# Kernel optimization log

Measured on AMD Instinct MI355X. Metric: run time of the kernel, lower is better.

The kernel has to match this reference:

```python
import jax, jax.numpy as jnp
import numpy as np

S, B, D, H = 512, 32, 1024, 16
HD = D // H
EPS = 1e-5


def layer_norm(x, w, b):
    xf = x.astype(jnp.float32)
    mu = jnp.mean(xf, axis=-1, keepdims=True)
    var = jnp.mean(jnp.square(xf - mu), axis=-1, keepdims=True)
    return ((xf - mu) * jax.lax.rsqrt(var + EPS) * w + b).astype(x.dtype)


def quick_gelu(x):
    return x * jax.nn.sigmoid(1.702 * x)


def setup_inputs() -> dict:
    key = jax.random.key(0)
    ks = jax.random.split(key, 6)
    sc = 0.02
    return {
        "x": jax.random.normal(ks[0], (S, B, D), dtype=jnp.float32),
        "ln1_w": jnp.ones((D,), jnp.float32),
        "ln1_b": jnp.zeros((D,), jnp.float32),
        "in_proj_w": jax.random.normal(ks[1], (3 * D, D), jnp.float32) * sc,
        "in_proj_b": jnp.zeros((3 * D,), jnp.float32),
        "out_w": jax.random.normal(ks[2], (D, D), jnp.float32) * sc,
        "out_b": jnp.zeros((D,), jnp.float32),
        "ln2_w": jnp.ones((D,), jnp.float32),
        "ln2_b": jnp.zeros((D,), jnp.float32),
        "fc_w": jax.random.normal(ks[3], (4 * D, D), jnp.float32) * sc,
        "fc_b": jnp.zeros((4 * D,), jnp.float32),
        "proj_w": jax.random.normal(ks[4], (D, 4 * D), jnp.float32) * sc,
        "proj_b": jnp.zeros((D,), jnp.float32),
    }


def reference(x, ln1_w, ln1_b, in_proj_w, in_proj_b, out_w, out_b,
              ln2_w, ln2_b, fc_w, fc_b, proj_w, proj_b):
    # ---- MHA on ln_1(x) (torch eager path, need_weights=True) ----
    h = layer_norm(x, ln1_w, ln1_b)                      # (S,B,D)
    qkv = h @ in_proj_w.T + in_proj_b                    # (S,B,3D)
    q, k, v = jnp.split(qkv, 3, axis=-1)
    # (S,B,D) -> (B,H,S,hd)
    def to_bhsd(t):
        return t.reshape(S, B, H, HD).transpose(1, 2, 0, 3)
    q, k, v = to_bhsd(q), to_bhsd(k), to_bhsd(v)
    scores = jnp.einsum('bhqd,bhkd->bhqk', q, k) / jnp.sqrt(jnp.float32(HD))
    attn = jax.nn.softmax(scores, axis=-1)               # (B,H,S,S)
    attn_weights = jnp.mean(attn, axis=1)                # avg over heads: (B,S,S)
    ctx = jnp.einsum('bhqk,bhkd->bhqd', attn, v)         # (B,H,S,hd)
    ctx = ctx.transpose(2, 0, 1, 3).reshape(S, B, D)     # (S,B,D)
    attn_out = ctx @ out_w.T + out_b
    x = x + attn_out
    # ---- MLP on ln_2(x) ----
    m = layer_norm(x, ln2_w, ln2_b)
    m = quick_gelu(m @ fc_w.T + fc_b)
    x = x + (m @ proj_w.T + proj_b)
    return x, attn_weights
```

## Files before the change

### kernel.cpp

```cpp
#include <hip/hip_runtime.h>
#include <hip/hip_bf16.h>

typedef __bf16 bf16x8 __attribute__((ext_vector_type(8)));
typedef __bf16 bf16x4 __attribute__((ext_vector_type(4)));
typedef float f32x4 __attribute__((ext_vector_type(4)));

#define SEQ 512
#define BATCH 32
#define DIM 1024
#define NHEAD 16
#define MROWS (SEQ * BATCH)

__device__ __forceinline__ void gload16(const void* g, void* s) {
    __builtin_amdgcn_global_load_lds((const __attribute__((address_space(1))) void*)g,
                                     (__attribute__((address_space(3))) void*)s, 16, 0, 0);
}

__device__ __forceinline__ f32x4 mfma16(bf16x8 a, bf16x8 b, f32x4 c) {
    return __builtin_amdgcn_mfma_f32_16x16x32_bf16(a, b, c, 0, 0, 0);
}

__global__ __launch_bounds__(256) void cvt_kernel(const float* __restrict__ src,
                                                  __bf16* __restrict__ dst, int n) {
    int i = (blockIdx.x * 256 + threadIdx.x) * 4;
    if (i < n) {
        float4 v = *(const float4*)(src + i);
        bf16x4 o;
        o[0] = (__bf16)v.x; o[1] = (__bf16)v.y; o[2] = (__bf16)v.z; o[3] = (__bf16)v.w;
        *(bf16x4*)&dst[i] = o;
    }
}

__global__ __launch_bounds__(256) void ln_kernel(const float* __restrict__ x,
                                                 const float* __restrict__ w,
                                                 const float* __restrict__ b,
                                                 __bf16* __restrict__ out) {
    int row = blockIdx.x, t = threadIdx.x;
    const float4* xr = (const float4*)(x + (size_t)row * DIM);
    float4 v = xr[t];
    float s  = v.x + v.y + v.z + v.w;
    float ss = v.x * v.x + v.y * v.y + v.z * v.z + v.w * v.w;
#pragma unroll
    for (int o = 1; o < 64; o <<= 1) { s += __shfl_xor(s, o); ss += __shfl_xor(ss, o); }
    __shared__ float red[8];
    if ((t & 63) == 0) { red[t >> 6] = s; red[4 + (t >> 6)] = ss; }
    __syncthreads();
    s  = red[0] + red[1] + red[2] + red[3];
    ss = red[4] + red[5] + red[6] + red[7];
    float mu = s * (1.f / DIM);
    float rs = rsqrtf(ss * (1.f / DIM) - mu * mu + 1e-5f);
    int c = t * 4;
    bf16x4 o4;
    o4[0] = (__bf16)((v.x - mu) * rs * w[c + 0] + b[c + 0]);
    o4[1] = (__bf16)((v.y - mu) * rs * w[c + 1] + b[c + 1]);
    o4[2] = (__bf16)((v.z - mu) * rs * w[c + 2] + b[c + 2]);
    o4[3] = (__bf16)((v.w - mu) * rs * w[c + 3] + b[c + 3]);
    *(bf16x4*)&out[(size_t)row * DIM + c] = o4;
}

template <int MODE>
__global__ __launch_bounds__(256) void gemm_kernel(const __bf16* __restrict__ A,
                                                   const __bf16* __restrict__ W,
                                                   const float* __restrict__ bias,
                                                   const float* res, void* out,
                                                   int M, int N, int K) {
    __shared__ __bf16 As[128 * 64];
    __shared__ __bf16 Bs[128 * 64];
    char* Ab_s = (char*)As;
    char* Bb_s = (char*)Bs;
    int t = threadIdx.x, l = t & 63, wv = t >> 6;
    int m0 = blockIdx.y * 128, n0 = blockIdx.x * 128;
    int wm = (wv >> 1) * 64, wn = (wv & 1) * 64;
    int lr = l & 15, lqb = (l >> 4) * 16;
    f32x4 acc[4][4];
#pragma unroll
    for (int i = 0; i < 4; i++)
#pragma unroll
        for (int j = 0; j < 4; j++) acc[i][j] = (f32x4){0.f, 0.f, 0.f, 0.f};

    const __bf16* Ag = A + (size_t)m0 * K;
    const __bf16* Wg = W + (size_t)n0 * K;
    int srow = t >> 3, sslot = t & 7;

    for (int k0 = 0; k0 < K; k0 += 64) {
#pragma unroll
        for (int it = 0; it < 4; ++it) {
            int row = it * 32 + srow;
            int col = (sslot ^ (row & 7)) * 8;
            int L = it * 4096 + t * 16;
            gload16(Ag + (size_t)row * K + k0 + col, Ab_s + L);
            gload16(Wg + (size_t)row * K + k0 + col, Bb_s + L);
        }
        __syncthreads();
#pragma unroll
        for (int f2 = 0; f2 < 2; ++f2) {
            bf16x8 af[4], bfr[4];
#pragma unroll
            for (int i = 0; i < 4; i++) {
                int row = wm + i * 16 + lr;
                af[i] = *(const bf16x8*)(Ab_s + row * 128 + ((f2 * 64 + lqb) ^ ((row & 7) << 4)));
            }
#pragma unroll
            for (int j = 0; j < 4; j++) {
                int row = wn + j * 16 + lr;
                bfr[j] = *(const bf16x8*)(Bb_s + row * 128 + ((f2 * 64 + lqb) ^ ((row & 7) << 4)));
            }
#pragma unroll
            for (int i = 0; i < 4; i++)
#pragma unroll
                for (int j = 0; j < 4; j++)
                    acc[i][j] = mfma16(af[i], bfr[j], acc[i][j]);
        }
        __syncthreads();
    }

#pragma unroll
    for (int j = 0; j < 4; j++) {
        int col = n0 + wn + j * 16 + lr;
        float bv = bias[col];
#pragma unroll
        for (int i = 0; i < 4; i++) {
#pragma unroll
            for (int r = 0; r < 4; r++) {
                int row = m0 + wm + i * 16 + (l >> 4) * 4 + r;
                float v = acc[i][j][r] + bv;
                if (MODE == 1) v = v / (1.f + __expf(-1.702f * v));
                size_t idx = (size_t)row * N + col;
                if (MODE == 2) ((float*)out)[idx] = v + res[idx];
                else           ((__bf16*)out)[idx] = (__bf16)v;
            }
        }
    }
}

__global__ __launch_bounds__(256) void vtr_kernel(const __bf16* __restrict__ qkv,
                                                  __bf16* __restrict__ Vt) {
    __shared__ __bf16 tl[64 * 72];
    char* tb = (char*)tl;
    int t = threadIdx.x;
    int bh = blockIdx.x >> 3, st = blockIdx.x & 7;
    int bb = bh >> 4, h = bh & 15;
#pragma unroll
    for (int it = 0; it < 2; ++it) {
        int s = it * 32 + (t >> 3), d0 = (t & 7) * 8;
        bf16x8 v = *(const bf16x8*)&qkv[((size_t)((st * 64 + s) * BATCH + bb)) * 3072 + 2048 + h * 64 + d0];
        *(bf16x8*)(tb + s * 144 + ((d0 * 2) ^ (((s + (s >> 3)) & 7) << 4))) = v;
    }
    __syncthreads();
#pragma unroll
    for (int it = 0; it < 2; ++it) {
        int d = it * 32 + (t >> 3), s0 = (t & 7) * 8;
        bf16x8 o;
#pragma unroll
        for (int e = 0; e < 8; ++e) {
            int s = s0 + e;
            o[e] = *(const __bf16*)(tb + s * 144 + ((d * 2) ^ (((s + (s >> 3)) & 7) << 4)));
        }
        *(bf16x8*)&Vt[((size_t)(bb * NHEAD + h) * 64 + d) * 512 + st * 64 + s0] = o;
    }
}

__global__ __launch_bounds__(512, 4) void attn_kernel(const __bf16* __restrict__ qkv,
                                                      const __bf16* __restrict__ Vt,
                                                      __bf16* __restrict__ ctx,
                                                      float* __restrict__ attnw) {
    __shared__ __bf16 kvbuf[16384];
    __shared__ __bf16 p16s[16384];
    __shared__ __bf16 qts[2048];
    __shared__ float redm[32][4];
    __shared__ float reds[32][4];
    char* kvb = (char*)kvbuf;
    char* pps = (char*)p16s;
    char* qtb = (char*)qts;

    const int t = threadIdx.x;
    const int l = t & 63, w = t >> 6;
    const int wq = w >> 2, wc = w & 3;
    const int lq = l >> 4, lr = l & 15;
    const int bb = blockIdx.x & 31;
    const int qt0 = blockIdx.x >> 5;

    const int ksl = t >> 3, kslot = t & 7;
    const int vdl = t >> 5, vslot = t & 31;

    float aw[8][4];
#pragma unroll
    for (int i = 0; i < 8; i++)
#pragma unroll
        for (int r = 0; r < 4; r++) aw[i][r] = 0.f;

    const int prow = wq * 16 + lr;
    const int vd = wc * 16 + lr;

    for (int h = 0; h < NHEAD; ++h) {
        if (t < 256) {
            int qr = t >> 3, slot = t & 7;
            int d0 = (slot ^ (qr & 7)) * 8;
            gload16(qkv + ((size_t)((qt0 * 32 + qr) * BATCH + bb)) * 3072 + h * 64 + d0,
                    qtb + t * 16);
        }
#pragma unroll
        for (int it = 0; it < 4; ++it) {
            int s = it * 64 + ksl;
            int d0 = (kslot ^ (s & 7)) * 8;
            gload16(qkv + ((size_t)(s * BATCH + bb)) * 3072 + 1024 + h * 64 + d0,
                    kvb + it * 8192 + t * 16);
        }
        __syncthreads();

        bf16x8 af0 = *(const bf16x8*)(qtb + prow * 128 + ((lq * 16) ^ ((prow & 7) << 4)));
        bf16x8 af1 = *(const bf16x8*)(qtb + prow * 128 + ((64 + lq * 16) ^ ((prow & 7) << 4)));

        f32x4 acc[8];
#pragma unroll
        for (int i = 0; i < 8; i++) acc[i] = (f32x4){0.f, 0.f, 0.f, 0.f};

#pragma unroll
        for (int ntl = 0; ntl < 4; ++ntl) {
            int r = wc * 64 + ntl * 16 + lr;
            bf16x8 b0 = *(const bf16x8*)(kvb + r * 128 + ((lq * 16) ^ ((r & 7) << 4)));
            bf16x8 b1 = *(const bf16x8*)(kvb + r * 128 + ((64 + lq * 16) ^ ((r & 7) << 4)));
            acc[ntl] = mfma16(af0, b0, acc[ntl]);
            acc[ntl] = mfma16(af1, b1, acc[ntl]);
        }
        __syncthreads();
#pragma unroll
        for (int it = 0; it < 4; ++it) {
            int s = it * 64 + ksl;
            int d0 = (kslot ^ (s & 7)) * 8;
            gload16(qkv + ((size_t)((256 + s) * BATCH + bb)) * 3072 + 1024 + h * 64 + d0,
                    kvb + it * 8192 + t * 16);
        }
        __syncthreads();
#pragma unroll
        for (int ntl = 0; ntl < 4; ++ntl) {
            int r = wc * 64 + ntl * 16 + lr;
            bf16x8 b0 = *(const bf16x8*)(kvb + r * 128 + ((lq * 16) ^ ((r & 7) << 4)));
            bf16x8 b1 = *(const bf16x8*)(kvb + r * 128 + ((64 + lq * 16) ^ ((r & 7) << 4)));
            acc[4 + ntl] = mfma16(af0, b0, acc[4 + ntl]);
            acc[4 + ntl] = mfma16(af1, b1, acc[4 + ntl]);
        }
        __syncthreads();
#pragma unroll
        for (int it = 0; it < 4; ++it) {
            int d = it * 16 + vdl;
            int s0 = (vslot ^ (d & 7)) * 8;
            gload16(Vt + ((size_t)(bb * NHEAD + h) * 64 + d) * 512 + s0,
                    kvb + it * 8192 + t * 16);
        }
#pragma unroll
        for (int i = 0; i < 8; i++) acc[i] *= 0.125f;
        float mx[4];
#pragma unroll
        for (int r = 0; r < 4; ++r) {
            float m = acc[0][r];
#pragma unroll
            for (int i = 1; i < 8; ++i) m = fmaxf(m, acc[i][r]);
#pragma unroll
            for (int o = 1; o < 16; o <<= 1) m = fmaxf(m, __shfl_xor(m, o));
            mx[r] = m;
        }
        if (lr == 0) {
            redm[wq * 16 + lq * 4 + 0][wc] = mx[0];
            redm[wq * 16 + lq * 4 + 1][wc] = mx[1];
            redm[wq * 16 + lq * 4 + 2][wc] = mx[2];
            redm[wq * 16 + lq * 4 + 3][wc] = mx[3];
        }
        __syncthreads();
        float g[4], sm[4];
#pragma unroll
        for (int r = 0; r < 4; ++r) {
            int row = wq * 16 + lq * 4 + r;
            g[r] = fmaxf(fmaxf(redm[row][0], redm[row][1]),
                         fmaxf(redm[row][2], redm[row][3]));
            sm[r] = 0.f;
        }
#pragma unroll
        for (int i = 0; i < 8; ++i)
#pragma unroll
            for (int r = 0; r < 4; ++r) {
                float p = __expf(acc[i][r] - g[r]);
                acc[i][r] = p;
                sm[r] += p;
            }
#pragma unroll
        for (int r = 0; r < 4; ++r)
#pragma unroll
            for (int o = 1; o < 16; o <<= 1) sm[r] += __shfl_xor(sm[r], o);
        if (lr == 0) {
            reds[wq * 16 + lq * 4 + 0][wc] = sm[0];
            reds[wq * 16 + lq * 4 + 1][wc] = sm[1];
            reds[wq * 16 + lq * 4 + 2][wc] = sm[2];
            reds[wq * 16 + lq * 4 + 3][wc] = sm[3];
        }
        __syncthreads();
        float inv[4];
#pragma unroll
        for (int r = 0; r < 4; ++r) {
            int row = wq * 16 + lq * 4 + r;
            inv[r] = 1.f / (reds[row][0] + reds[row][1] + reds[row][2] + reds[row][3]);
        }
#pragma unroll
        for (int i = 0; i < 8; ++i) {
#pragma unroll
            for (int r = 0; r < 4; ++r) {
                float pn = acc[i][r] * inv[r];
                aw[i][r] += pn;
                int row = wq * 16 + lq * 4 + r;
                int cbyte = (i >> 2) * 512 + wc * 128 + (i & 3) * 32 + lr * 2;
                *(__bf16*)(pps + row * 1024 + (cbyte ^ ((row & 7) << 4))) = (__bf16)pn;
            }
        }
        __syncthreads();
        f32x4 cacc = (f32x4){0.f, 0.f, 0.f, 0.f};
#pragma unroll
        for (int ks = 0; ks < 8; ++ks) {
            bf16x8 ap = *(const bf16x8*)(pps + prow * 1024 + ((ks * 64 + lq * 16) ^ ((prow & 7) << 4)));
            bf16x8 bv = *(const bf16x8*)(kvb + vd * 512 + ((ks * 64 + lq * 16) ^ ((vd & 7) << 4)));
            cacc = mfma16(ap, bv, cacc);
        }
        __syncthreads();
#pragma unroll
        for (int it = 0; it < 4; ++it) {
            int d = it * 16 + vdl;
            int s0 = (vslot ^ (d & 7)) * 8;
            gload16(Vt + ((size_t)(bb * NHEAD + h) * 64 + d) * 512 + 256 + s0,
                    kvb + it * 8192 + t * 16);
        }
        __syncthreads();
#pragma unroll
        for (int ks = 0; ks < 8; ++ks) {
            bf16x8 ap = *(const bf16x8*)(pps + prow * 1024 + ((512 + ks * 64 + lq * 16) ^ ((prow & 7) << 4)));
            bf16x8 bv = *(const bf16x8*)(kvb + vd * 512 + ((ks * 64 + lq * 16) ^ ((vd & 7) << 4)));
            cacc = mfma16(ap, bv, cacc);
        }
#pragma unroll
        for (int r = 0; r < 4; ++r) {
            int q = qt0 * 32 + wq * 16 + lq * 4 + r;
            ctx[((size_t)(q * BATCH + bb)) * DIM + h * 64 + wc * 16 + lr] = (__bf16)cacc[r];
        }
        __syncthreads();
    }
#pragma unroll
    for (int i = 0; i < 8; ++i)
#pragma unroll
        for (int r = 0; r < 4; ++r) {
            int q = qt0 * 32 + wq * 16 + lq * 4 + r;
            int col = (i >> 2) * 256 + wc * 64 + (i & 3) * 16 + lr;
            attnw[(size_t)bb * (SEQ * SEQ) + (size_t)q * SEQ + col] = aw[i][r] * (1.f / NHEAD);
        }
}

extern "C" void kernel_launch(void* const* d_in, const int* in_sizes, int n_in,
                              void* d_out, int out_size, void* d_ws, size_t ws_size,
                              hipStream_t stream) {
    const float* x    = (const float*)d_in[0];
    const float* ln1w = (const float*)d_in[1];
    const float* ln1b = (const float*)d_in[2];
    const float* ipw  = (const float*)d_in[3];
    const float* ipb  = (const float*)d_in[4];
    const float* outw = (const float*)d_in[5];
    const float* outb = (const float*)d_in[6];
    const float* ln2w = (const float*)d_in[7];
    const float* ln2b = (const float*)d_in[8];
    const float* fcw  = (const float*)d_in[9];
    const float* fcb  = (const float*)d_in[10];
    const float* pjw  = (const float*)d_in[11];
    const float* pjb  = (const float*)d_in[12];

    float* xout  = (float*)d_out;
    float* awout = xout + (size_t)MROWS * DIM;

    __bf16* wip   = (__bf16*)d_ws;
    __bf16* wout_ = wip + 3145728;
    __bf16* wfc   = wout_ + 1048576;
    __bf16* wpj   = wfc + 4194304;
    __bf16* hbuf  = wpj + 4194304;
    __bf16* big   = hbuf + (size_t)MROWS * DIM;
    __bf16* qkv   = big;
    __bf16* ctxb  = big + (size_t)MROWS * 3072;
    __bf16* mg    = big;
    __bf16* Vt    = hbuf;

    cvt_kernel<<<3072, 256, 0, stream>>>(ipw,  wip,   3145728);
    cvt_kernel<<<1024, 256, 0, stream>>>(outw, wout_, 1048576);
    cvt_kernel<<<4096, 256, 0, stream>>>(fcw,  wfc,   4194304);
    cvt_kernel<<<4096, 256, 0, stream>>>(pjw,  wpj,   4194304);

    ln_kernel<<<MROWS, 256, 0, stream>>>(x, ln1w, ln1b, hbuf);

    gemm_kernel<0><<<dim3(24, 128), 256, 0, stream>>>(hbuf, wip, ipb, nullptr, qkv,
                                                      MROWS, 3072, 1024);

    vtr_kernel<<<32 * 16 * 8, 256, 0, stream>>>(qkv, Vt);

    attn_kernel<<<512, 512, 0, stream>>>(qkv, Vt, ctxb, awout);

    gemm_kernel<2><<<dim3(8, 128), 256, 0, stream>>>(ctxb, wout_, outb, x, xout,
                                                     MROWS, 1024, 1024);

    ln_kernel<<<MROWS, 256, 0, stream>>>(xout, ln2w, ln2b, hbuf);

    gemm_kernel<1><<<dim3(32, 128), 256, 0, stream>>>(hbuf, wfc, fcb, nullptr, mg,
                                                      MROWS, 4096, 1024);

    gemm_kernel<2><<<dim3(8, 128), 256, 0, stream>>>(mg, wpj, pjb, xout, xout,
                                                     MROWS, 1024, 4096);
}
```

Before: 1.211 ms.

## Replace GEMM with 256x256 double-buffered 8-wave pipelined kernel

Replaces the 128x128 single-buffered GEMM with a 256x256-tile, 512-thread kernel. It double-buffers LDS (128 KB) and interleaves async global-to-LDS loads with MFMA phases, using explicit waitcnt, barriers and setprio. Block indices are swizzled across XCD groups to improve L2 locality. This is meant to hide memory latency and raise MFMA utilisation in all four linear layers. In exchange it needs more registers, leaves fewer blocks per CU, and relies on hand-tuned synchronisation that could be fragile.

```diff
diff --git a/kernel.cpp b/kernel.cpp
--- a/kernel.cpp
+++ b/kernel.cpp
@@ -58,72 +58,210 @@
     *(bf16x4*)&out[(size_t)row * DIM + c] = o4;
 }
 
+#define BA0 0
+#define BB0 32768
+#define BA1 65536
+#define BB1 98304
+
+#define PH_MID \
+    __builtin_amdgcn_s_barrier(); \
+    asm volatile("s_waitcnt lgkmcnt(0)" ::: "memory"); \
+    __builtin_amdgcn_sched_barrier(0); \
+    __builtin_amdgcn_s_setprio(1);
+#define PH_END \
+    __builtin_amdgcn_s_setprio(0); \
+    __builtin_amdgcn_sched_barrier(0); \
+    __builtin_amdgcn_s_barrier();
+#define PH_END_VM4 \
+    __builtin_amdgcn_s_setprio(0); \
+    __builtin_amdgcn_sched_barrier(0); \
+    asm volatile("s_waitcnt vmcnt(4)" ::: "memory"); \
+    __builtin_amdgcn_s_barrier();
+#define PH_END_VM0 \
+    __builtin_amdgcn_s_setprio(0); \
+    __builtin_amdgcn_sched_barrier(0); \
+    asm volatile("s_waitcnt vmcnt(0)" ::: "memory"); \
+    __builtin_amdgcn_s_barrier();
+
 template <int MODE>
-__global__ __launch_bounds__(256) void gemm_kernel(const __bf16* __restrict__ A,
-                                                   const __bf16* __restrict__ W,
-                                                   const float* __restrict__ bias,
-                                                   const float* res, void* out,
-                                                   int M, int N, int K) {
-    __shared__ __bf16 As[128 * 64];
-    __shared__ __bf16 Bs[128 * 64];
-    char* Ab_s = (char*)As;
-    char* Bb_s = (char*)Bs;
-    int t = threadIdx.x, l = t & 63, wv = t >> 6;
-    int m0 = blockIdx.y * 128, n0 = blockIdx.x * 128;
-    int wm = (wv >> 1) * 64, wn = (wv & 1) * 64;
-    int lr = l & 15, lqb = (l >> 4) * 16;
-    f32x4 acc[4][4];
-#pragma unroll
-    for (int i = 0; i < 4; i++)
-#pragma unroll
-        for (int j = 0; j < 4; j++) acc[i][j] = (f32x4){0.f, 0.f, 0.f, 0.f};
-
-    const __bf16* Ag = A + (size_t)m0 * K;
-    const __bf16* Wg = W + (size_t)n0 * K;
-    int srow = t >> 3, sslot = t & 7;
-
-    for (int k0 = 0; k0 < K; k0 += 64) {
-#pragma unroll
-        for (int it = 0; it < 4; ++it) {
-            int row = it * 32 + srow;
-            int col = (sslot ^ (row & 7)) * 8;
-            int L = it * 4096 + t * 16;
-            gload16(Ag + (size_t)row * K + k0 + col, Ab_s + L);
-            gload16(Wg + (size_t)row * K + k0 + col, Bb_s + L);
-        }
-        __syncthreads();
-#pragma unroll
-        for (int f2 = 0; f2 < 2; ++f2) {
-            bf16x8 af[4], bfr[4];
-#pragma unroll
-            for (int i = 0; i < 4; i++) {
-                int row = wm + i * 16 + lr;
-                af[i] = *(const bf16x8*)(Ab_s + row * 128 + ((f2 * 64 + lqb) ^ ((row & 7) << 4)));
-            }
-#pragma unroll
-            for (int j = 0; j < 4; j++) {
-                int row = wn + j * 16 + lr;
-                bfr[j] = *(const bf16x8*)(Bb_s + row * 128 + ((f2 * 64 + lqb) ^ ((row & 7) << 4)));
-            }
-#pragma unroll
-            for (int i = 0; i < 4; i++)
-#pragma unroll
-                for (int j = 0; j < 4; j++)
-                    acc[i][j] = mfma16(af[i], bfr[j], acc[i][j]);
-        }
-        __syncthreads();
+__global__ __launch_bounds__(512, 2) void gemm8_kernel(const __bf16* __restrict__ A,
+                                                       const __bf16* __restrict__ W,
+                                                       const float* __restrict__ bias,
+                                                       const float* res, void* out,
+                                                       int M, int N, int K) {
+    __shared__ __align__(16) char lds[131072];
+    const int t = threadIdx.x, l = t & 63, wid = t >> 6;
+    const int wm = wid >> 2, wn = wid & 3;
+    const int lr = l & 15, lq = l >> 4;
+    const int kx = (lr & 7) << 4;
+
+    const int nwg = gridDim.x;
+    const int cpx = nwg >> 3;
+    const int swz = ((int)blockIdx.x & 7) * cpx + ((int)blockIdx.x >> 3);
+    const int MT = M >> 8;
+    const int nt = swz / MT, mt = swz - nt * MT;
+    const __bf16* Ag = A + ((size_t)mt << 8) * K;
+    const __bf16* Wg = W + ((size_t)nt << 8) * K;
+    const int NITER = K >> 7;
+
+    auto STAGE = [&](int dstbase, const __bf16* src, int half, int kt) {
+#pragma unroll
+        for (int i = 0; i < 2; ++i) {
+            int idx = i * 512 + t;
+            int r = idx >> 3, slot = idx & 7;
+            gload16(src + (size_t)(half * 128 + r) * K + kt * 64 + ((slot ^ (r & 7)) << 3),
+                    lds + dstbase + idx * 16);
+        }
+    };
+    auto LDA_ = [&](int base, int mi, int ks) -> bf16x8 {
+        int row = wm * 128 + mi * 16 + lr;
+        return *(const bf16x8*)(lds + base + row * 128 + ((ks * 64 + lq * 16) ^ kx));
+    };
+    auto LDB_ = [&](int base, int nj, int ks) -> bf16x8 {
+        int row = wn * 64 + nj * 16 + lr;
+        return *(const bf16x8*)(lds + base + row * 128 + ((ks * 64 + lq * 16) ^ kx));
+    };
+
+    f32x4 acc[8][4];
+#pragma unroll
+    for (int i = 0; i < 8; ++i)
+#pragma unroll
+        for (int j = 0; j < 4; ++j) acc[i][j] = (f32x4){0.f, 0.f, 0.f, 0.f};
+
+    STAGE(BB0, Wg, 0, 0); STAGE(BB0 + 16384, Wg, 1, 0);
+    STAGE(BA0, Ag, 0, 0); STAGE(BA0 + 16384, Ag, 1, 0);
+    STAGE(BB1, Wg, 0, 1); STAGE(BB1 + 16384, Wg, 1, 1);
+    asm volatile("s_waitcnt vmcnt(4)" ::: "memory");
+    __builtin_amdgcn_s_barrier();
+
+    for (int ki = 0; ki < NITER; ++ki) {
+        const int ks1 = 2 * ki + 1, ks2 = 2 * ki + 2, ks3 = 2 * ki + 3;
+        const bool st23 = (ki + 1 < NITER);
+        bf16x8 af[4][2], bfr[4][2];
+
+        __builtin_amdgcn_sched_barrier(0);
+#pragma unroll
+        for (int mi = 0; mi < 4; ++mi) { af[mi][0] = LDA_(BA0, mi, 0); af[mi][1] = LDA_(BA0, mi, 1); }
+#pragma unroll
+        for (int nj = 0; nj < 2; ++nj) { bfr[nj][0] = LDB_(BB0, nj, 0); bfr[nj][1] = LDB_(BB0, nj, 1); }
+        STAGE(BA1, Ag, 0, ks1);
+        PH_MID
+#pragma unroll
+        for (int mi = 0; mi < 4; ++mi)
+#pragma unroll
+            for (int nj = 0; nj < 2; ++nj) {
+                acc[mi][nj] = mfma16(af[mi][0], bfr[nj][0], acc[mi][nj]);
+                acc[mi][nj] = mfma16(af[mi][1], bfr[nj][1], acc[mi][nj]);
+            }
+        PH_END
+
+        __builtin_amdgcn_sched_barrier(0);
+#pragma unroll
+        for (int nj = 2; nj < 4; ++nj) { bfr[nj][0] = LDB_(BB0, nj, 0); bfr[nj][1] = LDB_(BB0, nj, 1); }
+        STAGE(BA1 + 16384, Ag, 1, ks1);
+        PH_MID
+#pragma unroll
+        for (int mi = 0; mi < 4; ++mi)
+#pragma unroll
+            for (int nj = 2; nj < 4; ++nj) {
+                acc[mi][nj] = mfma16(af[mi][0], bfr[nj][0], acc[mi][nj]);
+                acc[mi][nj] = mfma16(af[mi][1], bfr[nj][1], acc[mi][nj]);
+            }
+        PH_END
+
+        __builtin_amdgcn_sched_barrier(0);
+#pragma unroll
+        for (int m = 0; m < 4; ++m) { af[m][0] = LDA_(BA0, m + 4, 0); af[m][1] = LDA_(BA0, m + 4, 1); }
+        if (st23) STAGE(BB0, Wg, 0, ks2);
+        PH_MID
+#pragma unroll
+        for (int m = 0; m < 4; ++m)
+#pragma unroll
+            for (int nj = 0; nj < 2; ++nj) {
+                acc[m + 4][nj] = mfma16(af[m][0], bfr[nj][0], acc[m + 4][nj]);
+                acc[m + 4][nj] = mfma16(af[m][1], bfr[nj][1], acc[m + 4][nj]);
+            }
+        PH_END
+
+        __builtin_amdgcn_sched_barrier(0);
+        if (st23) STAGE(BB0 + 16384, Wg, 1, ks2);
+        PH_MID
+#pragma unroll
+        for (int m = 0; m < 4; ++m)
+#pragma unroll
+            for (int nj = 2; nj < 4; ++nj) {
+                acc[m + 4][nj] = mfma16(af[m][0], bfr[nj][0], acc[m + 4][nj]);
+                acc[m + 4][nj] = mfma16(af[m][1], bfr[nj][1], acc[m + 4][nj]);
+            }
+        if (st23) { PH_END_VM4 } else { PH_END_VM0 }
+
+        __builtin_amdgcn_sched_barrier(0);
+#pragma unroll
+        for (int mi = 0; mi < 4; ++mi) { af[mi][0] = LDA_(BA1, mi, 0); af[mi][1] = LDA_(BA1, mi, 1); }
+#pragma unroll
+        for (int nj = 0; nj < 2; ++nj) { bfr[nj][0] = LDB_(BB1, nj, 0); bfr[nj][1] = LDB_(BB1, nj, 1); }
+        if (st23) STAGE(BA0, Ag, 0, ks2);
+        PH_MID
+#pragma unroll
+        for (int mi = 0; mi < 4; ++mi)
+#pragma unroll
+            for (int nj = 0; nj < 2; ++nj) {
+                acc[mi][nj] = mfma16(af[mi][0], bfr[nj][0], acc[mi][nj]);
+                acc[mi][nj] = mfma16(af[mi][1], bfr[nj][1], acc[mi][nj]);
+            }
+        PH_END
+
+        __builtin_amdgcn_sched_barrier(0);
+#pragma unroll
+        for (int nj = 2; nj < 4; ++nj) { bfr[nj][0] = LDB_(BB1, nj, 0); bfr[nj][1] = LDB_(BB1, nj, 1); }
+        if (st23) STAGE(BA0 + 16384, Ag, 1, ks2);
+        PH_MID
+#pragma unroll
+        for (int mi = 0; mi < 4; ++mi)
+#pragma unroll
+            for (int nj = 2; nj < 4; ++nj) {
+                acc[mi][nj] = mfma16(af[mi][0], bfr[nj][0], acc[mi][nj]);
+                acc[mi][nj] = mfma16(af[mi][1], bfr[nj][1], acc[mi][nj]);
+            }
+        PH_END
+
+        __builtin_amdgcn_sched_barrier(0);
+#pragma unroll
+        for (int m = 0; m < 4; ++m) { af[m][0] = LDA_(BA1, m + 4, 0); af[m][1] = LDA_(BA1, m + 4, 1); }
+        if (st23) STAGE(BB1, Wg, 0, ks3);
+        PH_MID
+#pragma unroll
+        for (int m = 0; m < 4; ++m)
+#pragma unroll
+            for (int nj = 0; nj < 2; ++nj) {
+                acc[m + 4][nj] = mfma16(af[m][0], bfr[nj][0], acc[m + 4][nj]);
+                acc[m + 4][nj] = mfma16(af[m][1], bfr[nj][1], acc[m + 4][nj]);
+            }
+        PH_END
+
+        __builtin_amdgcn_sched_barrier(0);
+        if (st23) STAGE(BB1 + 16384, Wg, 1, ks3);
+        PH_MID
+#pragma unroll
+        for (int m = 0; m < 4; ++m)
+#pragma unroll
+            for (int nj = 2; nj < 4; ++nj) {
+                acc[m + 4][nj] = mfma16(af[m][0], bfr[nj][0], acc[m + 4][nj]);
+                acc[m + 4][nj] = mfma16(af[m][1], bfr[nj][1], acc[m + 4][nj]);
+            }
+        PH_END_VM4
     }
 
 #pragma unroll
-    for (int j = 0; j < 4; j++) {
-        int col = n0 + wn + j * 16 + lr;
+    for (int nj = 0; nj < 4; ++nj) {
+        int col = (nt << 8) + wn * 64 + nj * 16 + lr;
         float bv = bias[col];
 #pragma unroll
-        for (int i = 0; i < 4; i++) {
-#pragma unroll
-            for (int r = 0; r < 4; r++) {
-                int row = m0 + wm + i * 16 + (l >> 4) * 4 + r;
-                float v = acc[i][j][r] + bv;
+        for (int mi = 0; mi < 8; ++mi) {
+#pragma unroll
+            for (int r = 0; r < 4; ++r) {
+                int row = (mt << 8) + wm * 128 + mi * 16 + lq * 4 + r;
+                float v = acc[mi][nj][r] + bv;
                 if (MODE == 1) v = v / (1.f + __expf(-1.702f * v));
                 size_t idx = (size_t)row * N + col;
                 if (MODE == 2) ((float*)out)[idx] = v + res[idx];
@@ -389,21 +527,21 @@
 
     ln_kernel<<<MROWS, 256, 0, stream>>>(x, ln1w, ln1b, hbuf);
 
-    gemm_kernel<0><<<dim3(24, 128), 256, 0, stream>>>(hbuf, wip, ipb, nullptr, qkv,
-                                                      MROWS, 3072, 1024);
+    gemm8_kernel<0><<<64 * 12, 512, 0, stream>>>(hbuf, wip, ipb, nullptr, qkv,
+                                                 MROWS, 3072, 1024);
 
     vtr_kernel<<<32 * 16 * 8, 256, 0, stream>>>(qkv, Vt);
 
     attn_kernel<<<512, 512, 0, stream>>>(qkv, Vt, ctxb, awout);
 
-    gemm_kernel<2><<<dim3(8, 128), 256, 0, stream>>>(ctxb, wout_, outb, x, xout,
-                                                     MROWS, 1024, 1024);
+    gemm8_kernel<2><<<64 * 4, 512, 0, stream>>>(ctxb, wout_, outb, x, xout,
+                                                MROWS, 1024, 1024);
 
     ln_kernel<<<MROWS, 256, 0, stream>>>(xout, ln2w, ln2b, hbuf);
 
-    gemm_kernel<1><<<dim3(32, 128), 256, 0, stream>>>(hbuf, wfc, fcb, nullptr, mg,
-                                                      MROWS, 4096, 1024);
-
-    gemm_kernel<2><<<dim3(8, 128), 256, 0, stream>>>(mg, wpj, pjb, xout, xout,
-                                                     MROWS, 1024, 4096);
-}
+    gemm8_kernel<1><<<64 * 16, 512, 0, stream>>>(hbuf, wfc, fcb, nullptr, mg,
+                                                 MROWS, 4096, 1024);
+
+    gemm8_kernel<2><<<64 * 4, 512, 0, stream>>>(mg, wpj, pjb, xout, xout,
+                                                MROWS, 1024, 4096);
+}
```

After: 1.107 ms. 1.09x faster.
